# Performance work log

Measured on AMD Instinct MI355X. Metric: run time of the kernel, lower is better.

The kernel has to match this reference:

```python
import jax, jax.numpy as jnp
import numpy as np

B, N, S, D, H = 8, 64, 128, 512, 8
DK = D // H


def setup_inputs() -> dict:
    key = jax.random.key(0)
    ks = jax.random.split(key, 8)
    x = jax.random.normal(ks[0], (B, N, S, D), dtype=jnp.float32)
    mask = jax.random.randint(ks[1], (B, N, S), 0, 2).astype(jnp.int32)
    mask = mask.at[..., 0].set(1)  # guarantee at least one valid token per sentence
    w = 1.0 / np.sqrt(D).astype(np.float32)
    Wq = jax.random.normal(ks[2], (D, D), dtype=jnp.float32) * w
    Wk = jax.random.normal(ks[3], (D, D), dtype=jnp.float32) * w
    Wv = jax.random.normal(ks[4], (D, D), dtype=jnp.float32) * w
    Wo = jax.random.normal(ks[5], (D, D), dtype=jnp.float32) * w
    bq = jnp.zeros((D,), jnp.float32)
    bk = jnp.zeros((D,), jnp.float32)
    bv = jnp.zeros((D,), jnp.float32)
    bo = jnp.zeros((D,), jnp.float32)
    sent_q = jax.random.normal(ks[6], (H, DK), dtype=jnp.float32)
    return {"x": x, "mask": mask, "Wq": Wq, "bq": bq, "Wk": Wk, "bk": bk,
            "Wv": Wv, "bv": bv, "sent_q": sent_q, "Wo": Wo, "bo": bo}


def reference(x, mask, Wq, bq, Wk, bk, Wv, bv, sent_q, Wo, bo):
    b, n, s, d = x.shape
    h, dk = sent_q.shape
    inv_sqrt_dk = 1.0 / np.sqrt(dk).astype(np.float32)
    # QKV projections, split heads: (B, N, S, H, dk)
    Q = (x @ Wq + bq).reshape(b, n, s, h, dk)
    K = (x @ Wk + bk).reshape(b, n, s, h, dk)
    V = (x @ Wv + bv).reshape(b, n, s, h, dk)
    # sentence-query attention over tokens within each sentence: (B, H, N, S)
    sent_scores = jnp.einsum('hd,bnshd->bhns', sent_q, K) * inv_sqrt_dk
    sent_scores = jnp.where(mask[:, None, :, :] == 0, jnp.float32(-1e9), sent_scores)
    sent_attn = jax.nn.softmax(sent_scores, axis=-1)
    # pooled per-sentence representation: (B, H, N, dk)
    sent_repr = jnp.einsum('bhns,bnshd->bhnd', sent_attn, V)
    # degenerate token softmax over a single key (== 1), kept faithfully
    token_scores = jnp.einsum('bnshd,bhnd->bhns', Q, sent_repr) * inv_sqrt_dk
    token_attn = jax.nn.softmax(token_scores[..., None], axis=-1)[..., 0]  # (B,H,N,S), all ones
    # broadcast pooled repr to every token, scale by (unit) attn: (B, H, N, S, dk)
    out = token_attn[..., None] * sent_repr[:, :, :, None, :]
    out = jnp.transpose(out, (0, 2, 3, 1, 4)).reshape(b, n, s, d)
    return out @ Wo + bo
```

## Files before the change

### kernel.cpp

```cpp
#include <hip/hip_runtime.h>
#include <math.h>

#define BB 8
#define NN 64
#define SS 128
#define DD 512
#define HH 8
#define DKK 64

__global__ void precompute_wk(const float* __restrict__ Wk,
                              const float* __restrict__ sq,
                              float* __restrict__ wk_t) {
    const int d = threadIdx.x;
    const int h = blockIdx.x;
    const float4* wrow = (const float4*)(Wk + (size_t)d * DD + h * DKK);
    const float4* sqv  = (const float4*)(sq + h * DKK);
    float acc = 0.f;
#pragma unroll
    for (int k = 0; k < DKK / 4; ++k) {
        float4 w = wrow[k], q = sqv[k];
        acc += w.x * q.x + w.y * q.y + w.z * q.z + w.w * q.w;
    }
    wk_t[h * DD + d] = acc;
}

__global__ __launch_bounds__(512, 4)
void sent_attn_kernel(const float* __restrict__ x,
                      const int* __restrict__ mask,
                      const float* __restrict__ wk_t,
                      const float* __restrict__ Wv,
                      const float* __restrict__ bv,
                      const float* __restrict__ Wo,
                      const float* __restrict__ bo,
                      float* __restrict__ out) {
    __shared__ float sc[HH][SS];
    __shared__ float xbar[HH][DD];
    __shared__ float zsh[DD];

    const int bid  = blockIdx.x;
    const int t    = threadIdx.x;
    const int wave = t >> 6;
    const int lane = t & 63;
    const float* xt = x + (size_t)bid * SS * DD;

    const int d0 = lane * 8;
    float4 wkA[HH], wkB[HH];
#pragma unroll
    for (int h = 0; h < HH; ++h) {
        wkA[h] = *(const float4*)(wk_t + h * DD + d0);
        wkB[h] = *(const float4*)(wk_t + h * DD + d0 + 4);
    }

    for (int s = wave; s < SS; s += 8) {
        const float* xr = xt + s * DD + d0;
        float4 xa = *(const float4*)xr;
        float4 xb = *(const float4*)(xr + 4);
        float p[HH];
#pragma unroll
        for (int h = 0; h < HH; ++h) {
            p[h] = xa.x * wkA[h].x + xa.y * wkA[h].y + xa.z * wkA[h].z + xa.w * wkA[h].w
                 + xb.x * wkB[h].x + xb.y * wkB[h].y + xb.z * wkB[h].z + xb.w * wkB[h].w;
        }
#pragma unroll
        for (int off = 32; off > 0; off >>= 1) {
#pragma unroll
            for (int h = 0; h < HH; ++h)
                p[h] += __shfl_down(p[h], off, 64);
        }
        if (lane == 0) {
            const int m = mask[bid * SS + s];
#pragma unroll
            for (int h = 0; h < HH; ++h)
                sc[h][s] = (m == 0) ? -1e9f : p[h] * 0.125f;
        }
    }
    __syncthreads();

    {
        const int h = wave;
        float v0 = sc[h][lane], v1 = sc[h][lane + 64];
        float m = fmaxf(v0, v1);
#pragma unroll
        for (int off = 32; off > 0; off >>= 1)
            m = fmaxf(m, __shfl_xor(m, off, 64));
        float e0 = __expf(v0 - m);
        float e1 = __expf(v1 - m);
        float ssum = e0 + e1;
#pragma unroll
        for (int off = 32; off > 0; off >>= 1)
            ssum += __shfl_xor(ssum, off, 64);
        float inv = 1.0f / ssum;
        sc[h][lane]      = e0 * inv;
        sc[h][lane + 64] = e1 * inv;
    }
    __syncthreads();

    {
        float acc[HH];
#pragma unroll
        for (int h = 0; h < HH; ++h) acc[h] = 0.f;
#pragma unroll 4
        for (int s = 0; s < SS; ++s) {
            float xv = xt[(size_t)s * DD + t];
#pragma unroll
            for (int h = 0; h < HH; ++h)
                acc[h] += sc[h][s] * xv;
        }
#pragma unroll
        for (int h = 0; h < HH; ++h) xbar[h][t] = acc[h];
    }
    __syncthreads();

    {
        const int h = t >> 6;
        const float* wvp = Wv + t;
        const float* xb  = &xbar[h][0];
        float a0 = 0.f, a1 = 0.f, a2 = 0.f, a3 = 0.f;
#pragma unroll 4
        for (int d = 0; d < DD; d += 4) {
            a0 += xb[d + 0] * wvp[(size_t)(d + 0) * DD];
            a1 += xb[d + 1] * wvp[(size_t)(d + 1) * DD];
            a2 += xb[d + 2] * wvp[(size_t)(d + 2) * DD];
            a3 += xb[d + 3] * wvp[(size_t)(d + 3) * DD];
        }
        zsh[t] = bv[t] + ((a0 + a1) + (a2 + a3));
    }
    __syncthreads();

    {
        const float* wop = Wo + t;
        float a0 = 0.f, a1 = 0.f, a2 = 0.f, a3 = 0.f;
#pragma unroll 4
        for (int d = 0; d < DD; d += 4) {
            a0 += zsh[d + 0] * wop[(size_t)(d + 0) * DD];
            a1 += zsh[d + 1] * wop[(size_t)(d + 1) * DD];
            a2 += zsh[d + 2] * wop[(size_t)(d + 2) * DD];
            a3 += zsh[d + 3] * wop[(size_t)(d + 3) * DD];
        }
        const float y = bo[t] + ((a0 + a1) + (a2 + a3));
        float* op = out + (size_t)bid * SS * DD + t;
#pragma unroll 4
        for (int s = 0; s < SS; ++s)
            op[(size_t)s * DD] = y;
    }
}

extern "C" void kernel_launch(void* const* d_in, const int* in_sizes, int n_in,
                              void* d_out, int out_size, void* d_ws, size_t ws_size,
                              hipStream_t stream) {
    const float* x    = (const float*)d_in[0];
    const int*   mask = (const int*)  d_in[1];
    const float* Wk   = (const float*)d_in[4];
    const float* Wv   = (const float*)d_in[6];
    const float* bv   = (const float*)d_in[7];
    const float* sq   = (const float*)d_in[8];
    const float* Wo   = (const float*)d_in[9];
    const float* bo   = (const float*)d_in[10];
    float* out  = (float*)d_out;
    float* wk_t = (float*)d_ws;

    precompute_wk<<<HH, DD, 0, stream>>>(Wk, sq, wk_t);
    sent_attn_kernel<<<BB * NN, DD, 0, stream>>>(x, mask, wk_t, Wv, bv, Wo, bo, out);
}
```

Measured before the change: 118.6 us.

## Split fused sentence-attention kernel into staged kernels with batched tiled GEMMs

```diff
diff --git a/kernel.cpp b/kernel.cpp
--- a/kernel.cpp
+++ b/kernel.cpp
@@ -7,6 +7,13 @@
 #define DD 512
 #define HH 8
 #define DKK 64
+#define NSENT (BB * NN)
+#define SENT_STRIDE (SS * DD)
+
+#define Y_OFF  0
+#define Z_OFF  DD
+#define XB_OFF (2 * DD)
+#define W_OFF  (10 * DD)
 
 __global__ void precompute_wk(const float* __restrict__ Wk,
                               const float* __restrict__ sq,
@@ -24,24 +31,13 @@
     wk_t[h * DD + d] = acc;
 }
 
-__global__ __launch_bounds__(512, 4)
-void sent_attn_kernel(const float* __restrict__ x,
-                      const int* __restrict__ mask,
-                      const float* __restrict__ wk_t,
-                      const float* __restrict__ Wv,
-                      const float* __restrict__ bv,
-                      const float* __restrict__ Wo,
-                      const float* __restrict__ bo,
-                      float* __restrict__ out) {
-    __shared__ float sc[HH][SS];
-    __shared__ float xbar[HH][DD];
-    __shared__ float zsh[DD];
-
-    const int bid  = blockIdx.x;
-    const int t    = threadIdx.x;
-    const int wave = t >> 6;
-    const int lane = t & 63;
-    const float* xt = x + (size_t)bid * SS * DD;
+__global__ __launch_bounds__(512)
+void kw_weights(const float* __restrict__ x, const int* __restrict__ mask,
+                const float* __restrict__ wk_t, float* __restrict__ outp)
+{
+    const int wave = threadIdx.x >> 6;
+    const int lane = threadIdx.x & 63;
+    const int tok0 = blockIdx.x * 64 + wave * 8;
 
     const int d0 = lane * 8;
     float4 wkA[HH], wkB[HH];
@@ -50,99 +46,165 @@
         wkA[h] = *(const float4*)(wk_t + h * DD + d0);
         wkB[h] = *(const float4*)(wk_t + h * DD + d0 + 4);
     }
-
-    for (int s = wave; s < SS; s += 8) {
-        const float* xr = xt + s * DD + d0;
+    const int hsel = lane & 7;
+
+#pragma unroll 2
+    for (int j = 0; j < 8; ++j) {
+        const int tok = tok0 + j;
+        const int m = mask[tok];
+        const float* xr = x + (size_t)tok * DD + d0;
         float4 xa = *(const float4*)xr;
         float4 xb = *(const float4*)(xr + 4);
         float p[HH];
 #pragma unroll
-        for (int h = 0; h < HH; ++h) {
+        for (int h = 0; h < HH; ++h)
             p[h] = xa.x * wkA[h].x + xa.y * wkA[h].y + xa.z * wkA[h].z + xa.w * wkA[h].w
                  + xb.x * wkB[h].x + xb.y * wkB[h].y + xb.z * wkB[h].z + xb.w * wkB[h].w;
+#pragma unroll
+        for (int off = 1; off <= 4; off <<= 1)
+#pragma unroll
+            for (int h = 0; h < HH; ++h)
+                p[h] += __shfl_xor(p[h], off, 64);
+        float v = p[0];
+#pragma unroll
+        for (int h = 1; h < HH; ++h) v = (hsel == h) ? p[h] : v;
+        v += __shfl_xor(v, 8, 64);
+        v += __shfl_xor(v, 16, 64);
+        v += __shfl_xor(v, 32, 64);
+        if (lane < HH) {
+            const float e = m ? __expf(v * 0.125f) : 0.f;
+            const int sent = tok >> 7, s = tok & (SS - 1);
+            outp[(size_t)sent * SENT_STRIDE + W_OFF + hsel * SS + s] = e;
         }
-#pragma unroll
-        for (int off = 32; off > 0; off >>= 1) {
-#pragma unroll
-            for (int h = 0; h < HH; ++h)
-                p[h] += __shfl_down(p[h], off, 64);
+    }
+}
+
+__global__ __launch_bounds__(256)
+void kx_xbar(const float* __restrict__ x, float* __restrict__ outp)
+{
+    __shared__ float wl[HH * SS];
+    __shared__ float rsh[HH];
+
+    const int bid  = blockIdx.x;
+    const int sent = bid >> 1, half = bid & 1;
+    const int t    = threadIdx.x;
+    float* base = outp + (size_t)sent * SENT_STRIDE;
+
+    float4 wv = *(const float4*)(base + W_OFF + t * 4);
+    *(float4*)&wl[t * 4] = wv;
+    float ps = wv.x + wv.y + wv.z + wv.w;
+#pragma unroll
+    for (int off = 1; off <= 16; off <<= 1)
+        ps += __shfl_xor(ps, off, 64);
+    if ((t & 31) == 0) rsh[t >> 5] = 1.0f / ps;
+    __syncthreads();
+
+    const int d = half * 256 + t;
+    const float* xp = x + (size_t)sent * SENT_STRIDE + d;
+    float acc[HH];
+#pragma unroll
+    for (int h = 0; h < HH; ++h) acc[h] = 0.f;
+
+#pragma unroll 4
+    for (int s0 = 0; s0 < SS; s0 += 4) {
+        const float x0 = xp[(size_t)(s0 + 0) * DD];
+        const float x1 = xp[(size_t)(s0 + 1) * DD];
+        const float x2 = xp[(size_t)(s0 + 2) * DD];
+        const float x3 = xp[(size_t)(s0 + 3) * DD];
+#pragma unroll
+        for (int h = 0; h < HH; ++h) {
+            const float4 w4 = *(const float4*)&wl[h * SS + s0];
+            acc[h] += w4.x * x0 + w4.y * x1 + w4.z * x2 + w4.w * x3;
         }
-        if (lane == 0) {
-            const int m = mask[bid * SS + s];
-#pragma unroll
-            for (int h = 0; h < HH; ++h)
-                sc[h][s] = (m == 0) ? -1e9f : p[h] * 0.125f;
+    }
+#pragma unroll
+    for (int h = 0; h < HH; ++h)
+        base[XB_OFF + h * DD + d] = acc[h] * rsh[h];
+}
+
+__global__ __launch_bounds__(256)
+void gemm_proj(const float* __restrict__ A, const int a_nb_stride,
+               const float* __restrict__ B, const float* __restrict__ bias,
+               float* __restrict__ C)
+{
+    __shared__ float Ast[64][33];
+    __shared__ float Bs[64][68];
+
+    const int bid = blockIdx.x;
+    const int nb = bid & 7, mb = bid >> 3;
+    const int t  = threadIdx.x;
+    const int tr = t >> 4, tc = t & 15;
+    const int lr = t >> 3, lkq = t & 7;
+    const int bkr = t >> 2, bcq = t & 3;
+
+    const float* Ab = A + (size_t)(mb * 32) * SENT_STRIDE + nb * a_nb_stride;
+    const float* Bb = B + nb * 64;
+
+    float ac[2][4];
+#pragma unroll
+    for (int i = 0; i < 2; ++i)
+#pragma unroll
+        for (int j = 0; j < 4; ++j) ac[i][j] = 0.f;
+
+    for (int k0 = 0; k0 < DD; k0 += 64) {
+        const float* ap = Ab + (size_t)lr * SENT_STRIDE + k0 + lkq * 8;
+        float4 a0 = *(const float4*)(ap);
+        float4 a1 = *(const float4*)(ap + 4);
+        const float* bp = Bb + (size_t)(k0 + bkr) * DD + bcq * 16;
+        float4 b0 = *(const float4*)(bp + 0);
+        float4 b1 = *(const float4*)(bp + 4);
+        float4 b2 = *(const float4*)(bp + 8);
+        float4 b3 = *(const float4*)(bp + 12);
+        __syncthreads();
+        Ast[lkq * 8 + 0][lr] = a0.x;
+        Ast[lkq * 8 + 1][lr] = a0.y;
+        Ast[lkq * 8 + 2][lr] = a0.z;
+        Ast[lkq * 8 + 3][lr] = a0.w;
+        Ast[lkq * 8 + 4][lr] = a1.x;
+        Ast[lkq * 8 + 5][lr] = a1.y;
+        Ast[lkq * 8 + 6][lr] = a1.z;
+        Ast[lkq * 8 + 7][lr] = a1.w;
+        *(float4*)&Bs[bkr][bcq * 16 + 0]  = b0;
+        *(float4*)&Bs[bkr][bcq * 16 + 4]  = b1;
+        *(float4*)&Bs[bkr][bcq * 16 + 8]  = b2;
+        *(float4*)&Bs[bkr][bcq * 16 + 12] = b3;
+        __syncthreads();
+#pragma unroll
+        for (int kk = 0; kk < 64; ++kk) {
+            const float a_0 = Ast[kk][tr * 2 + 0];
+            const float a_1 = Ast[kk][tr * 2 + 1];
+            const float4 b4 = *(const float4*)&Bs[kk][tc * 4];
+            ac[0][0] += a_0 * b4.x; ac[0][1] += a_0 * b4.y;
+            ac[0][2] += a_0 * b4.z; ac[0][3] += a_0 * b4.w;
+            ac[1][0] += a_1 * b4.x; ac[1][1] += a_1 * b4.y;
+            ac[1][2] += a_1 * b4.z; ac[1][3] += a_1 * b4.w;
         }
     }
-    __syncthreads();
-
-    {
-        const int h = wave;
-        float v0 = sc[h][lane], v1 = sc[h][lane + 64];
-        float m = fmaxf(v0, v1);
-#pragma unroll
-        for (int off = 32; off > 0; off >>= 1)
-            m = fmaxf(m, __shfl_xor(m, off, 64));
-        float e0 = __expf(v0 - m);
-        float e1 = __expf(v1 - m);
-        float ssum = e0 + e1;
-#pragma unroll
-        for (int off = 32; off > 0; off >>= 1)
-            ssum += __shfl_xor(ssum, off, 64);
-        float inv = 1.0f / ssum;
-        sc[h][lane]      = e0 * inv;
-        sc[h][lane + 64] = e1 * inv;
-    }
-    __syncthreads();
-
-    {
-        float acc[HH];
-#pragma unroll
-        for (int h = 0; h < HH; ++h) acc[h] = 0.f;
-#pragma unroll 4
-        for (int s = 0; s < SS; ++s) {
-            float xv = xt[(size_t)s * DD + t];
-#pragma unroll
-            for (int h = 0; h < HH; ++h)
-                acc[h] += sc[h][s] * xv;
-        }
-#pragma unroll
-        for (int h = 0; h < HH; ++h) xbar[h][t] = acc[h];
-    }
-    __syncthreads();
-
-    {
-        const int h = t >> 6;
-        const float* wvp = Wv + t;
-        const float* xb  = &xbar[h][0];
-        float a0 = 0.f, a1 = 0.f, a2 = 0.f, a3 = 0.f;
-#pragma unroll 4
-        for (int d = 0; d < DD; d += 4) {
-            a0 += xb[d + 0] * wvp[(size_t)(d + 0) * DD];
-            a1 += xb[d + 1] * wvp[(size_t)(d + 1) * DD];
-            a2 += xb[d + 2] * wvp[(size_t)(d + 2) * DD];
-            a3 += xb[d + 3] * wvp[(size_t)(d + 3) * DD];
-        }
-        zsh[t] = bv[t] + ((a0 + a1) + (a2 + a3));
-    }
-    __syncthreads();
-
-    {
-        const float* wop = Wo + t;
-        float a0 = 0.f, a1 = 0.f, a2 = 0.f, a3 = 0.f;
-#pragma unroll 4
-        for (int d = 0; d < DD; d += 4) {
-            a0 += zsh[d + 0] * wop[(size_t)(d + 0) * DD];
-            a1 += zsh[d + 1] * wop[(size_t)(d + 1) * DD];
-            a2 += zsh[d + 2] * wop[(size_t)(d + 2) * DD];
-            a3 += zsh[d + 3] * wop[(size_t)(d + 3) * DD];
-        }
-        const float y = bo[t] + ((a0 + a1) + (a2 + a3));
-        float* op = out + (size_t)bid * SS * DD + t;
-#pragma unroll 4
-        for (int s = 0; s < SS; ++s)
-            op[(size_t)s * DD] = y;
-    }
+
+    const float4 bb = *(const float4*)(bias + nb * 64 + tc * 4);
+#pragma unroll
+    for (int i = 0; i < 2; ++i) {
+        float4 o;
+        o.x = ac[i][0] + bb.x;
+        o.y = ac[i][1] + bb.y;
+        o.z = ac[i][2] + bb.z;
+        o.w = ac[i][3] + bb.w;
+        *(float4*)(C + (size_t)(mb * 32 + tr * 2 + i) * SENT_STRIDE + nb * 64 + tc * 4) = o;
+    }
+}
+
+__global__ __launch_bounds__(256)
+void kb_bcast(float* __restrict__ outp)
+{
+    const int sent = blockIdx.x >> 3, q = blockIdx.x & 7;
+    float* base = outp + (size_t)sent * SENT_STRIDE;
+    const int c  = threadIdx.x & 127;
+    const int rh = threadIdx.x >> 7;
+    const float4 y = *(const float4*)(base + c * 4);
+    float* w0 = base + (size_t)(q * 16 + rh) * DD + c * 4;
+#pragma unroll
+    for (int i = 0; i < 8; ++i)
+        *(float4*)(w0 + (size_t)(i * 2) * DD) = y;
 }
 
 extern "C" void kernel_launch(void* const* d_in, const int* in_sizes, int n_in,
@@ -160,5 +222,9 @@
     float* wk_t = (float*)d_ws;
 
     precompute_wk<<<HH, DD, 0, stream>>>(Wk, sq, wk_t);
-    sent_attn_kernel<<<BB * NN, DD, 0, stream>>>(x, mask, wk_t, Wv, bv, Wo, bo, out);
-}
+    kw_weights<<<(BB * NN * SS) / 64, 512, 0, stream>>>(x, mask, wk_t, out);
+    kx_xbar<<<NSENT * 2, 256, 0, stream>>>(x, out);
+    gemm_proj<<<128, 256, 0, stream>>>(out + XB_OFF, DD, Wv, bv, out + Z_OFF);
+    gemm_proj<<<128, 256, 0, stream>>>(out + Z_OFF, 0, Wo, bo, out + Y_OFF);
+    kb_bcast<<<NSENT * 8, 256, 0, stream>>>(out);
+}
```

After: 123.4 us. +4.1%, slower.

## Split fused sentence kernel into pooling, tiled GEMMs, and broadcast kernels

Applied to the files above, without the earlier changes.

```diff
diff --git a/kernel.cpp b/kernel.cpp
--- a/kernel.cpp
+++ b/kernel.cpp
@@ -7,6 +7,13 @@
 #define DD 512
 #define HH 8
 #define DKK 64
+#define NSENT (BB * NN)
+#define SENT_STRIDE (SS * DD)
+
+#define WK_OFF 0
+#define XB_OFF 4096
+#define Z_OFF  (XB_OFF + NSENT * HH * DD)
+#define YY_OFF (Z_OFF + NSENT * DD)
 
 __global__ void precompute_wk(const float* __restrict__ Wk,
                               const float* __restrict__ sq,
@@ -24,24 +31,18 @@
     wk_t[h * DD + d] = acc;
 }
 
-__global__ __launch_bounds__(512, 4)
-void sent_attn_kernel(const float* __restrict__ x,
-                      const int* __restrict__ mask,
-                      const float* __restrict__ wk_t,
-                      const float* __restrict__ Wv,
-                      const float* __restrict__ bv,
-                      const float* __restrict__ Wo,
-                      const float* __restrict__ bo,
-                      float* __restrict__ out) {
-    __shared__ float sc[HH][SS];
-    __shared__ float xbar[HH][DD];
-    __shared__ float zsh[DD];
-
-    const int bid  = blockIdx.x;
+__global__ __launch_bounds__(512)
+void ka_xbar(const float* __restrict__ x, const int* __restrict__ mask,
+             const float* __restrict__ wk_t, float* __restrict__ xbar)
+{
+    __shared__ float wl[HH][SS];
+    __shared__ float rsh[HH];
+
+    const int sent = blockIdx.x;
     const int t    = threadIdx.x;
     const int wave = t >> 6;
     const int lane = t & 63;
-    const float* xt = x + (size_t)bid * SS * DD;
+    const float* xs = x + (size_t)sent * SENT_STRIDE;
 
     const int d0 = lane * 8;
     float4 wkA[HH], wkB[HH];
@@ -50,99 +51,164 @@
         wkA[h] = *(const float4*)(wk_t + h * DD + d0);
         wkB[h] = *(const float4*)(wk_t + h * DD + d0 + 4);
     }
-
-    for (int s = wave; s < SS; s += 8) {
-        const float* xr = xt + s * DD + d0;
-        float4 xa = *(const float4*)xr;
-        float4 xb = *(const float4*)(xr + 4);
-        float p[HH];
+    const int hsel = lane & 7;
+
+    for (int j = 0; j < 16; j += 2) {
+        const int s0 = wave * 16 + j;
+        const float* xr0 = xs + (size_t)s0 * DD + d0;
+        const float* xr1 = xr0 + DD;
+        float4 xa0 = *(const float4*)xr0;
+        float4 xb0 = *(const float4*)(xr0 + 4);
+        float4 xa1 = *(const float4*)xr1;
+        float4 xb1 = *(const float4*)(xr1 + 4);
+        const int m0 = mask[sent * SS + s0];
+        const int m1 = mask[sent * SS + s0 + 1];
+        float p0[HH], p1[HH];
 #pragma unroll
         for (int h = 0; h < HH; ++h) {
-            p[h] = xa.x * wkA[h].x + xa.y * wkA[h].y + xa.z * wkA[h].z + xa.w * wkA[h].w
-                 + xb.x * wkB[h].x + xb.y * wkB[h].y + xb.z * wkB[h].z + xb.w * wkB[h].w;
-        }
-#pragma unroll
-        for (int off = 32; off > 0; off >>= 1) {
-#pragma unroll
-            for (int h = 0; h < HH; ++h)
-                p[h] += __shfl_down(p[h], off, 64);
-        }
-        if (lane == 0) {
-            const int m = mask[bid * SS + s];
-#pragma unroll
-            for (int h = 0; h < HH; ++h)
-                sc[h][s] = (m == 0) ? -1e9f : p[h] * 0.125f;
+            p0[h] = xa0.x * wkA[h].x + xa0.y * wkA[h].y + xa0.z * wkA[h].z + xa0.w * wkA[h].w
+                  + xb0.x * wkB[h].x + xb0.y * wkB[h].y + xb0.z * wkB[h].z + xb0.w * wkB[h].w;
+            p1[h] = xa1.x * wkA[h].x + xa1.y * wkA[h].y + xa1.z * wkA[h].z + xa1.w * wkA[h].w
+                  + xb1.x * wkB[h].x + xb1.y * wkB[h].y + xb1.z * wkB[h].z + xb1.w * wkB[h].w;
+        }
+#pragma unroll
+        for (int off = 1; off <= 4; off <<= 1) {
+#pragma unroll
+            for (int h = 0; h < HH; ++h) {
+                p0[h] += __shfl_xor(p0[h], off, 64);
+                p1[h] += __shfl_xor(p1[h], off, 64);
+            }
+        }
+        float v0 = p0[0], v1 = p1[0];
+#pragma unroll
+        for (int h = 1; h < HH; ++h) {
+            v0 = (hsel == h) ? p0[h] : v0;
+            v1 = (hsel == h) ? p1[h] : v1;
+        }
+#pragma unroll
+        for (int off = 8; off <= 32; off <<= 1) {
+            v0 += __shfl_xor(v0, off, 64);
+            v1 += __shfl_xor(v1, off, 64);
+        }
+        if (lane < HH) {
+            wl[lane][s0]     = m0 ? __expf(v0 * 0.125f) : 0.f;
+            wl[lane][s0 + 1] = m1 ? __expf(v1 * 0.125f) : 0.f;
         }
     }
     __syncthreads();
 
     {
-        const int h = wave;
-        float v0 = sc[h][lane], v1 = sc[h][lane + 64];
-        float m = fmaxf(v0, v1);
-#pragma unroll
-        for (int off = 32; off > 0; off >>= 1)
-            m = fmaxf(m, __shfl_xor(m, off, 64));
-        float e0 = __expf(v0 - m);
-        float e1 = __expf(v1 - m);
-        float ssum = e0 + e1;
-#pragma unroll
-        for (int off = 32; off > 0; off >>= 1)
-            ssum += __shfl_xor(ssum, off, 64);
-        float inv = 1.0f / ssum;
-        sc[h][lane]      = e0 * inv;
-        sc[h][lane + 64] = e1 * inv;
+        float v = wl[wave][lane] + wl[wave][lane + 64];
+#pragma unroll
+        for (int off = 1; off <= 32; off <<= 1)
+            v += __shfl_xor(v, off, 64);
+        if (lane == 0) rsh[wave] = 1.0f / v;
     }
     __syncthreads();
 
     {
+        const float* xp = xs + t;
         float acc[HH];
 #pragma unroll
         for (int h = 0; h < HH; ++h) acc[h] = 0.f;
-#pragma unroll 4
-        for (int s = 0; s < SS; ++s) {
-            float xv = xt[(size_t)s * DD + t];
-#pragma unroll
-            for (int h = 0; h < HH; ++h)
-                acc[h] += sc[h][s] * xv;
-        }
-#pragma unroll
-        for (int h = 0; h < HH; ++h) xbar[h][t] = acc[h];
-    }
-    __syncthreads();
-
-    {
-        const int h = t >> 6;
-        const float* wvp = Wv + t;
-        const float* xb  = &xbar[h][0];
-        float a0 = 0.f, a1 = 0.f, a2 = 0.f, a3 = 0.f;
-#pragma unroll 4
-        for (int d = 0; d < DD; d += 4) {
-            a0 += xb[d + 0] * wvp[(size_t)(d + 0) * DD];
-            a1 += xb[d + 1] * wvp[(size_t)(d + 1) * DD];
-            a2 += xb[d + 2] * wvp[(size_t)(d + 2) * DD];
-            a3 += xb[d + 3] * wvp[(size_t)(d + 3) * DD];
-        }
-        zsh[t] = bv[t] + ((a0 + a1) + (a2 + a3));
-    }
-    __syncthreads();
-
-    {
-        const float* wop = Wo + t;
-        float a0 = 0.f, a1 = 0.f, a2 = 0.f, a3 = 0.f;
-#pragma unroll 4
-        for (int d = 0; d < DD; d += 4) {
-            a0 += zsh[d + 0] * wop[(size_t)(d + 0) * DD];
-            a1 += zsh[d + 1] * wop[(size_t)(d + 1) * DD];
-            a2 += zsh[d + 2] * wop[(size_t)(d + 2) * DD];
-            a3 += zsh[d + 3] * wop[(size_t)(d + 3) * DD];
-        }
-        const float y = bo[t] + ((a0 + a1) + (a2 + a3));
-        float* op = out + (size_t)bid * SS * DD + t;
-#pragma unroll 4
-        for (int s = 0; s < SS; ++s)
-            op[(size_t)s * DD] = y;
-    }
+
+        float xa[8], xb[8];
+#pragma unroll
+        for (int j = 0; j < 8; ++j) xa[j] = xp[(size_t)j * DD];
+
+        for (int s0 = 0; s0 < SS; s0 += 16) {
+#pragma unroll
+            for (int j = 0; j < 8; ++j) xb[j] = xp[(size_t)(s0 + 8 + j) * DD];
+#pragma unroll
+            for (int j = 0; j < 8; ++j) {
+                const float xv = xa[j];
+#pragma unroll
+                for (int h = 0; h < HH; ++h) acc[h] += wl[h][s0 + j] * xv;
+            }
+            if (s0 + 16 < SS) {
+#pragma unroll
+                for (int j = 0; j < 8; ++j) xa[j] = xp[(size_t)(s0 + 16 + j) * DD];
+            }
+#pragma unroll
+            for (int j = 0; j < 8; ++j) {
+                const float xv = xb[j];
+#pragma unroll
+                for (int h = 0; h < HH; ++h) acc[h] += wl[h][s0 + 8 + j] * xv;
+            }
+        }
+        float* xbp = xbar + (size_t)sent * (HH * DD) + t;
+#pragma unroll
+        for (int h = 0; h < HH; ++h)
+            xbp[h * DD] = acc[h] * rsh[h];
+    }
+}
+
+__global__ __launch_bounds__(256)
+void gemm_tile(const float* __restrict__ A, const int am_stride, const int a_nb_stride,
+               const float* __restrict__ B, const float* __restrict__ bias,
+               float* __restrict__ C)
+{
+    __shared__ float As[64][17];
+    __shared__ float Bs[64][68];
+
+    const int nb = blockIdx.x & 7, mb = blockIdx.x >> 3;
+    const int t  = threadIdx.x;
+    const int tr = t >> 4, tc = t & 15;
+
+    const float* Ab = A + (size_t)(mb * 16) * am_stride + nb * a_nb_stride
+                        + (size_t)tr * am_stride + tc * 4;
+    const float* Bb = B + nb * 64 + (size_t)tr * DD + tc * 4;
+
+    float4 ar = *(const float4*)(Ab);
+    float4 br0 = *(const float4*)(Bb);
+    float4 br1 = *(const float4*)(Bb + 16 * DD);
+    float4 br2 = *(const float4*)(Bb + 32 * DD);
+    float4 br3 = *(const float4*)(Bb + 48 * DD);
+
+    float a0 = 0.f, a1 = 0.f, a2 = 0.f, a3 = 0.f;
+
+    for (int k0 = 0; k0 < DD; k0 += 64) {
+        As[tc * 4 + 0][tr] = ar.x;
+        As[tc * 4 + 1][tr] = ar.y;
+        As[tc * 4 + 2][tr] = ar.z;
+        As[tc * 4 + 3][tr] = ar.w;
+        *(float4*)&Bs[tr +  0][tc * 4] = br0;
+        *(float4*)&Bs[tr + 16][tc * 4] = br1;
+        *(float4*)&Bs[tr + 32][tc * 4] = br2;
+        *(float4*)&Bs[tr + 48][tc * 4] = br3;
+        __syncthreads();
+        if (k0 + 64 < DD) {
+            ar  = *(const float4*)(Ab + k0 + 64);
+            br0 = *(const float4*)(Bb + (size_t)(k0 + 64) * DD);
+            br1 = *(const float4*)(Bb + (size_t)(k0 + 80) * DD);
+            br2 = *(const float4*)(Bb + (size_t)(k0 + 96) * DD);
+            br3 = *(const float4*)(Bb + (size_t)(k0 + 112) * DD);
+        }
+#pragma unroll
+        for (int kk = 0; kk < 64; ++kk) {
+            const float av = As[kk][tr];
+            const float4 bv4 = *(const float4*)&Bs[kk][tc * 4];
+            a0 += av * bv4.x; a1 += av * bv4.y; a2 += av * bv4.z; a3 += av * bv4.w;
+        }
+        __syncthreads();
+    }
+
+    const float4 bb = *(const float4*)(bias + nb * 64 + tc * 4);
+    float4 o; o.x = a0 + bb.x; o.y = a1 + bb.y; o.z = a2 + bb.z; o.w = a3 + bb.w;
+    *(float4*)(C + (size_t)(mb * 16 + tr) * DD + nb * 64 + tc * 4) = o;
+}
+
+__global__ __launch_bounds__(256)
+void kb_bcast(const float* __restrict__ y, float* __restrict__ outp)
+{
+    const int sent = blockIdx.x >> 2, q = blockIdx.x & 3;
+    const int c4 = threadIdx.x & 127;
+    const int rr = threadIdx.x >> 7;
+    const float4 yv = *(const float4*)(y + (size_t)sent * DD + c4 * 4);
+    float* w0 = outp + (size_t)sent * SENT_STRIDE + (size_t)(q * 32 + rr) * DD + c4 * 4;
+#pragma unroll
+    for (int i = 0; i < 16; ++i)
+        *(float4*)(w0 + (size_t)(i * 2) * DD) = yv;
 }
 
 extern "C" void kernel_launch(void* const* d_in, const int* in_sizes, int n_in,
@@ -156,9 +222,17 @@
     const float* sq   = (const float*)d_in[8];
     const float* Wo   = (const float*)d_in[9];
     const float* bo   = (const float*)d_in[10];
-    float* out  = (float*)d_out;
-    float* wk_t = (float*)d_ws;
+    float* out = (float*)d_out;
+    float* ws  = (float*)d_ws;
+
+    float* wk_t = ws + WK_OFF;
+    float* xbar = ws + XB_OFF;
+    float* z    = ws + Z_OFF;
+    float* y    = ws + YY_OFF;
 
     precompute_wk<<<HH, DD, 0, stream>>>(Wk, sq, wk_t);
-    sent_attn_kernel<<<BB * NN, DD, 0, stream>>>(x, mask, wk_t, Wv, bv, Wo, bo, out);
-}
+    ka_xbar<<<NSENT, 512, 0, stream>>>(x, mask, wk_t, xbar);
+    gemm_tile<<<256, 256, 0, stream>>>(xbar, HH * DD, DD, Wv, bv, z);
+    gemm_tile<<<256, 256, 0, stream>>>(z, DD, 0, Wo, bo, y);
+    kb_bcast<<<NSENT * 4, 256, 0, stream>>>(y, out);
+}
```

After: 104.0 us (median of 5 runs). 1.14x faster.
